# Performance work log

Hardware: AMD Instinct MI355X
Metric: run time of the kernel (lower is better)

Reference implementation:

```python
import jax, jax.numpy as jnp
import numpy as np

N = 100_000   # nodes
E = 3_200_000 # edges (avg degree 32)
IN = 256      # input feature dim


def setup_inputs() -> dict:
    key = jax.random.key(0)
    ks = jax.random.split(key, 10)
    w = lambda k, s: (jax.random.normal(k, s, jnp.float32) * 0.02)
    return {
        "x": jax.random.normal(ks[0], (N, IN), jnp.float32),
        "edge_index": jax.random.randint(ks[1], (2, E), 0, N, dtype=jnp.int32),
        "edge_attr": jax.random.normal(ks[2], (E, 1), jnp.float32),
        # conv1: ExpGraphConv(IN, 64, 128)
        "W1a": w(ks[3], (IN, 64)), "b1a": jnp.zeros((64,), jnp.float32),
        "W1b": w(ks[4], (IN + 64, 128)), "b1b": jnp.zeros((128,), jnp.float32),
        # conv2: ExpGraphConv(128, 32->hidden 64? per ctor (128, 32, 64)): msg hidden 32... kept as repo: hidden=32? Using (128,64) msg, (192,64) out per faithful cat structure
        "W2a": w(ks[5], (128, 64)), "b2a": jnp.zeros((64,), jnp.float32),
        "W2b": w(ks[6], (128 + 64, 64)), "b2b": jnp.zeros((64,), jnp.float32),
        # head
        "Wl1": w(ks[7], (64, 32)), "bl1": jnp.zeros((32,), jnp.float32),
        "Wl2": w(ks[8], (32, 1)), "bl2": jnp.zeros((1,), jnp.float32),
    }


def _mean_aggr(h, src, dst, n):
    # gather messages from source nodes, scatter-mean into destination nodes
    s = jax.ops.segment_sum(h[src], dst, num_segments=n)          # [N, d]
    cnt = jax.ops.segment_sum(jnp.ones((src.shape[0],), h.dtype), dst, num_segments=n)
    return s / jnp.maximum(cnt, 1.0)[:, None]


def _exp_graph_conv(x, src, dst, Wa, ba, Wb, bb):
    # message MLP on source features, mean aggregation, then linear on [x || aggr]
    h = x @ Wa + ba                                               # [N, hidden]
    m = _mean_aggr(h, src, dst, x.shape[0])                       # [N, hidden]
    return jnp.concatenate([x, m], axis=1) @ Wb + bb              # [N, out]


def reference(x, edge_index, edge_attr, W1a, b1a, W1b, b1b, W2a, b2a, W2b, b2b, Wl1, bl1, Wl2, bl2):
    src, dst = edge_index[0], edge_index[1]
    x = jax.nn.relu(_exp_graph_conv(x, src, dst, W1a, b1a, W1b, b1b))
    x = jax.nn.relu(_exp_graph_conv(x, src, dst, W2a, b2a, W2b, b2b))
    x = jax.nn.relu(x @ Wl1 + bl1)
    return x @ Wl2 + bl2
```

## Files before the change

kernel.cpp:

```cpp
#include <hip/hip_runtime.h>
#include <type_traits>

#define IN_DIM 256
#define CAP 10240
#define EPB 4096

typedef _Float16 f16;
typedef _Float16 f16x8 __attribute__((ext_vector_type(8)));
typedef float f32x4 __attribute__((ext_vector_type(4)));
typedef unsigned u32x4 __attribute__((ext_vector_type(4)));
typedef unsigned u32x2 __attribute__((ext_vector_type(2)));


__global__ __launch_bounds__(256) void init_cur_k(int* __restrict__ bcur) {
    int i = blockIdx.x * 256 + threadIdx.x;
    if (i < 512) bcur[i] = i * CAP;
}

__global__ __launch_bounds__(256) void bucket_scatter_k(const int* __restrict__ srcp,
                                                        const int* __restrict__ dstp,
                                                        int* __restrict__ bcur,
                                                        unsigned* __restrict__ bedge, int E) {
    __shared__ int cnt[512], lstart[512], delta[512], fill[512];
    __shared__ int pfx[256];
    __shared__ unsigned spay[EPB];
    __shared__ unsigned char sbk[EPB];
    int tid = threadIdx.x;
    cnt[tid] = 0; cnt[tid + 256] = 0;
    fill[tid] = 0; fill[tid + 256] = 0;
    __syncthreads();
    size_t base = (size_t)blockIdx.x * EPB;
    int nloc = E - (int)base; if (nloc > EPB) nloc = EPB;
    int dreg[EPB / 256], sreg[EPB / 256];
#pragma unroll
    for (int j = 0; j < EPB / 256; j++) {
        int e = j * 256 + tid;
        if (e < nloc) {
            dreg[j] = dstp[base + e];
            sreg[j] = srcp[base + e];
            atomicAdd(&cnt[dreg[j] >> 8], 1);
        }
    }
    __syncthreads();
    int a0 = cnt[2 * tid], a1 = cnt[2 * tid + 1], s = a0 + a1;
    pfx[tid] = s;
    __syncthreads();
    for (int off = 1; off < 256; off <<= 1) {
        int t2 = (tid >= off) ? pfx[tid - off] : 0;
        __syncthreads();
        pfx[tid] += t2;
        __syncthreads();
    }
    int excl = pfx[tid] - s;
    lstart[2 * tid] = excl;
    lstart[2 * tid + 1] = excl + a0;
    int g0 = 0, g1 = 0;
    if (a0) g0 = atomicAdd(&bcur[2 * tid], a0);
    if (a1) g1 = atomicAdd(&bcur[2 * tid + 1], a1);
    delta[2 * tid] = g0 - excl;
    delta[2 * tid + 1] = g1 - (excl + a0);
    __syncthreads();
#pragma unroll
    for (int j = 0; j < EPB / 256; j++) {
        int e = j * 256 + tid;
        if (e < nloc) {
            int d = dreg[j], bk = d >> 8;
            int slot = lstart[bk] + atomicAdd(&fill[bk], 1);
            spay[slot] = (unsigned)sreg[j] | ((unsigned)(d & 255) << 17);
            sbk[slot] = (unsigned char)bk;
        }
    }
    __syncthreads();
    int mid = lstart[256];
#pragma unroll
    for (int j = 0; j < EPB / 256; j++) {
        int i = j * 256 + tid;
        if (i < nloc) {
            int bk = (int)sbk[i] | ((i >= mid) ? 256 : 0);
            int gp = i + delta[bk];
            if (gp < (bk + 1) * CAP)
                bedge[gp] = spay[i];
        }
    }
}

__global__ __launch_bounds__(256) void fine_sort_k(unsigned* __restrict__ bedge,
                                                   const int* __restrict__ bcur,
                                                   int2* __restrict__ ose, int Nn) {
    __shared__ int cnt[256], cur[256], pfx[256];
    __shared__ int sorted[CAP];
    int b = blockIdx.x, tid = threadIdx.x;
    int lo = b * CAP;
    int sz = bcur[b] - lo;
    if (sz > CAP) sz = CAP;
    cnt[tid] = 0;
    __syncthreads();
    for (int i = tid; i < sz; i += 256) atomicAdd(&cnt[bedge[lo + i] >> 17], 1);
    __syncthreads();
    int c = cnt[tid];
    pfx[tid] = c;
    __syncthreads();
    for (int off = 1; off < 256; off <<= 1) {
        int t2 = (tid >= off) ? pfx[tid - off] : 0;
        __syncthreads();
        pfx[tid] += t2;
        __syncthreads();
    }
    int excl = pfx[tid] - c;
    cur[tid] = excl;
    int node = b * 256 + tid;
    if (node < Nn) ose[node] = make_int2(lo + excl, lo + excl + c);
    __syncthreads();
    for (int i = tid; i < sz; i += 256) {
        unsigned v = bedge[lo + i];
        int slot = atomicAdd(&cur[v >> 17], 1);
        sorted[slot] = (int)(v & 0x1FFFFu);
    }
    __syncthreads();
    for (int i = tid; i < sz; i += 256) bedge[lo + i] = (unsigned)sorted[i];
}


__global__ __launch_bounds__(256) void castf16_k(const float* __restrict__ X,
                                                 f16* __restrict__ Y, int n4) {
    int i = blockIdx.x * 256 + threadIdx.x;
    if (i >= n4) return;
    f32x4 v = __builtin_nontemporal_load(reinterpret_cast<const f32x4*>(X) + i);
    union { f16 h[4]; u32x2 u; } p;
    p.h[0] = (f16)v.x; p.h[1] = (f16)v.y; p.h[2] = (f16)v.z; p.h[3] = (f16)v.w;
    __builtin_nontemporal_store(p.u, reinterpret_cast<u32x2*>(Y) + i);
}

__global__ __launch_bounds__(256) void wcast_k(const float* __restrict__ W,
                                               f16* __restrict__ Wt, int K, int N) {
    int i = blockIdx.x * 256 + threadIdx.x;
    if (i >= N * K) return;
    int n = i / K, k = i - n * K;
    Wt[i] = (f16)W[(size_t)k * N + n];
}


__global__ __launch_bounds__(256) void aggr_k(const int2* __restrict__ ose,
                                              const int* __restrict__ ssrc,
                                              const f16* __restrict__ h,
                                              f16* __restrict__ m, int n) {
    int wave = (blockIdx.x * 256 + threadIdx.x) >> 6;
    int lane = threadIdx.x & 63;
    if (wave >= n) return;
    int2 se = ose[wave];
    int s0 = se.x, s1 = se.y;
    int half = lane >> 5;
    int l32 = lane & 31;
    const unsigned* h32 = reinterpret_cast<const unsigned*>(h);
    float ax = 0.f, ay = 0.f;
    for (int c = s0; c < s1; c += 64) {
        int cn = min(64, s1 - c);
        int myidx = (lane < cn) ? ssrc[c + lane] : 0;
        int t = 0;
        for (; t + 8 <= cn; t += 8) {
            int ia = __shfl(myidx, t + 0 + half);
            int ib = __shfl(myidx, t + 2 + half);
            int ic = __shfl(myidx, t + 4 + half);
            int id = __shfl(myidx, t + 6 + half);
            unsigned ua = h32[(size_t)ia * 32 + l32];
            unsigned ub = h32[(size_t)ib * 32 + l32];
            unsigned uc = h32[(size_t)ic * 32 + l32];
            unsigned ud = h32[(size_t)id * 32 + l32];
            union { unsigned u; f16 hh[2]; } qa, qb, qc, qd;
            qa.u = ua; qb.u = ub; qc.u = uc; qd.u = ud;
            ax += (float)qa.hh[0] + (float)qb.hh[0] + (float)qc.hh[0] + (float)qd.hh[0];
            ay += (float)qa.hh[1] + (float)qb.hh[1] + (float)qc.hh[1] + (float)qd.hh[1];
        }
        for (; t + 2 <= cn; t += 2) {
            int ia = __shfl(myidx, t + half);
            unsigned ua = h32[(size_t)ia * 32 + l32];
            union { unsigned u; f16 hh[2]; } qa; qa.u = ua;
            ax += (float)qa.hh[0];
            ay += (float)qa.hh[1];
        }
        if (t < cn) {
            int ia = __shfl(myidx, t);
            if (half == 0) {
                unsigned ua = h32[(size_t)ia * 32 + l32];
                union { unsigned u; f16 hh[2]; } qa; qa.u = ua;
                ax += (float)qa.hh[0];
                ay += (float)qa.hh[1];
            }
        }
    }
    ax += __shfl_xor(ax, 32);
    ay += __shfl_xor(ay, 32);
    if (half == 0) {
        float inv = 1.0f / fmaxf((float)(s1 - s0), 1.0f);
        union { unsigned u; f16 hh[2]; } q;
        q.hh[0] = (f16)(ax * inv);
        q.hh[1] = (f16)(ay * inv);
        reinterpret_cast<unsigned*>(m + (size_t)wave * 64)[l32] = q.u;
    }
}


template <int BN, bool OUT_F16>
__global__ __launch_bounds__(256) void gemm_mfma(const f16* __restrict__ A1, int K1,
                                                 const f16* __restrict__ A2, int K2,
                                                 const f16* __restrict__ Wt,
                                                 const float* __restrict__ bias,
                                                 void* __restrict__ Yv, int M, int relu,
                                                 int stream_out) {
    constexpr int BM = 64, BK = 32;
    constexpr int WN = BN / 2;
    constexpr int NB = WN / 16;
    constexpr int SEGB = BN / 64;
    using T = typename std::conditional<OUT_F16, f16, float>::type;
    constexpr int EPS = BN + 8;
    constexpr int VECN = 16 / sizeof(T);
    constexpr int TPR = BN / VECN;
    constexpr size_t SM_AB = (size_t)BM * BK * 2 + (size_t)BN * BK * 2;
    constexpr size_t SM_EP = (size_t)BM * EPS * sizeof(T);
    constexpr size_t SM = SM_AB > SM_EP ? SM_AB : SM_EP;
    __shared__ __align__(16) char smem[SM];
    f16 (*As)[BK] = reinterpret_cast<f16(*)[BK]>(smem);
    f16 (*Bs)[BK] = reinterpret_cast<f16(*)[BK]>(smem + (size_t)BM * BK * 2);
    const int tid  = threadIdx.x;
    const int wave = tid >> 6;
    const int lane = tid & 63;
    const int wr   = wave >> 1;
    const int wc   = wave & 1;
    const int quad = lane >> 4;
    const int l16  = lane & 15;
    const int row0 = blockIdx.x * BM;
    const int Ktot = K1 + K2;

    f32x4 acc[2][NB];
#pragma unroll
    for (int i = 0; i < 2; i++)
#pragma unroll
        for (int j = 0; j < NB; j++) acc[i][j] = (f32x4)(0.f);

    const int ra = tid >> 2, sa = tid & 3;
    int rowA = row0 + ra;  if (rowA >= M) rowA = M - 1;

    u32x4 aReg, bReg[SEGB];
    auto loadA = [&](int kk) {
        const f16* base; int stride, kloc;
        if (kk < K1) { base = A1; stride = K1; kloc = kk; }
        else         { base = A2; stride = K2; kloc = kk - K1; }
        aReg = __builtin_nontemporal_load(
            reinterpret_cast<const u32x4*>(base + (size_t)rowA * stride + kloc + sa * 8));
    };
    auto loadB = [&](int kk) {
#pragma unroll
        for (int i = 0; i < SEGB; i++) {
            int fid = tid + i * 256;
            int n = fid >> 2, s = fid & 3;
            bReg[i] = *reinterpret_cast<const u32x4*>(Wt + (size_t)n * Ktot + kk + s * 8);
        }
    };

    loadA(0); loadB(0);
    for (int kk = 0; kk < Ktot; kk += BK) {
        reinterpret_cast<u32x4*>(&As[0][0])[tid] = aReg;
#pragma unroll
        for (int i = 0; i < SEGB; i++)
            reinterpret_cast<u32x4*>(&Bs[0][0])[tid + i * 256] = bReg[i];
        __syncthreads();
        if (kk + BK < Ktot) { loadA(kk + BK); loadB(kk + BK); }
        f16x8 af[2], bf[NB];
#pragma unroll
        for (int rb = 0; rb < 2; rb++) {
            int row = wr * 32 + rb * 16 + l16;
            af[rb] = *reinterpret_cast<const f16x8*>(&As[row][quad * 8]);
        }
#pragma unroll
        for (int cb = 0; cb < NB; cb++) {
            int n = wc * WN + cb * 16 + l16;
            bf[cb] = *reinterpret_cast<const f16x8*>(&Bs[n][quad * 8]);
        }
#pragma unroll
        for (int rb = 0; rb < 2; rb++)
#pragma unroll
            for (int cb = 0; cb < NB; cb++)
                acc[rb][cb] = __builtin_amdgcn_mfma_f32_16x16x32_f16(af[rb], bf[cb], acc[rb][cb], 0, 0, 0);
        __syncthreads();
    }

    T* ep = reinterpret_cast<T*>(smem);
#pragma unroll
    for (int rb = 0; rb < 2; rb++) {
#pragma unroll
        for (int cb = 0; cb < NB; cb++) {
            int col = wc * WN + cb * 16 + l16;
            float bv = bias[col];
#pragma unroll
            for (int r = 0; r < 4; r++) {
                int lrow = wr * 32 + rb * 16 + quad * 4 + r;
                float v = acc[rb][cb][r] + bv;
                if (relu) v = fmaxf(v, 0.f);
                ep[(size_t)lrow * EPS + col] = (T)v;
            }
        }
    }
    __syncthreads();
#pragma unroll
    for (int p = 0; p < BM * TPR / 256; p++) {
        int fid = p * 256 + tid;
        int row = fid / TPR, c = fid % TPR;
        int grow = row0 + row;
        if (grow < M) {
            u32x4 val = *reinterpret_cast<const u32x4*>(ep + (size_t)row * EPS + c * VECN);
            u32x4* dst = reinterpret_cast<u32x4*>((T*)Yv + (size_t)grow * BN + c * VECN);
            if (stream_out) __builtin_nontemporal_store(val, dst);
            else            *dst = val;
        }
    }
}


__global__ __launch_bounds__(256) void head_k(const f16* __restrict__ x2,
                                              const float* __restrict__ Wl1,
                                              const float* __restrict__ bl1,
                                              const float* __restrict__ Wl2,
                                              const float* __restrict__ bl2,
                                              float* __restrict__ out, int n) {
    __shared__ __align__(16) float w1[64 * 32];
    __shared__ float b1s[32];
    __shared__ float w2s[32];
    for (int t = threadIdx.x; t < 2048; t += 256) w1[t] = Wl1[t];
    if (threadIdx.x < 32) {
        b1s[threadIdx.x] = bl1[threadIdx.x];
        w2s[threadIdx.x] = Wl2[threadIdx.x];
    }
    __syncthreads();
    int i = blockIdx.x * 256 + threadIdx.x;
    if (i >= n) return;
    float v[64];
    const f16x8* xr = reinterpret_cast<const f16x8*>(x2 + (size_t)i * 64);
#pragma unroll
    for (int t = 0; t < 8; t++) {
        f16x8 q = xr[t];
#pragma unroll
        for (int j = 0; j < 8; j++) v[t * 8 + j] = (float)q[j];
    }
    float hj[32];
#pragma unroll
    for (int j = 0; j < 32; j++) hj[j] = b1s[j];
    for (int k = 0; k < 64; k++) {
        float vk = v[k];
        const float4* wrow = reinterpret_cast<const float4*>(&w1[k * 32]);
#pragma unroll
        for (int j4 = 0; j4 < 8; j4++) {
            float4 wq = wrow[j4];
            hj[j4 * 4 + 0] += vk * wq.x;
            hj[j4 * 4 + 1] += vk * wq.y;
            hj[j4 * 4 + 2] += vk * wq.z;
            hj[j4 * 4 + 3] += vk * wq.w;
        }
    }
    float o = bl2[0];
#pragma unroll
    for (int j = 0; j < 32; j++) o += fmaxf(hj[j], 0.f) * w2s[j];
    out[i] = o;
}


extern "C" void kernel_launch(void* const* d_in, const int* in_sizes, int n_in,
                              void* d_out, int out_size, void* d_ws, size_t ws_size,
                              hipStream_t stream) {
    const float* x   = (const float*)d_in[0];
    const int*   ei  = (const int*)d_in[1];
    const float* W1a = (const float*)d_in[3];
    const float* b1a = (const float*)d_in[4];
    const float* W1b = (const float*)d_in[5];
    const float* b1b = (const float*)d_in[6];
    const float* W2a = (const float*)d_in[7];
    const float* b2a = (const float*)d_in[8];
    const float* W2b = (const float*)d_in[9];
    const float* b2b = (const float*)d_in[10];
    const float* Wl1 = (const float*)d_in[11];
    const float* bl1 = (const float*)d_in[12];
    const float* Wl2 = (const float*)d_in[13];
    const float* bl2 = (const float*)d_in[14];

    const int N = in_sizes[0] / IN_DIM;
    const int E = in_sizes[1] / 2;
    const int* srcp = ei;
    const int* dstp = ei + E;

    char* ws = (char*)d_ws;
    size_t off = 0;
    auto alloc = [&](size_t bytes) -> char* {
        char* p = ws + off;
        off = (off + bytes + 255) & ~(size_t)255;
        return p;
    };
    int NB2 = (N + 255) / 256;
    int*      bcur  = (int*)alloc(512 * 4);
    unsigned* bedge = (unsigned*)alloc((size_t)NB2 * CAP * 4);
    int2*     ose   = (int2*)alloc((size_t)N * 8);
    f16*      x16   = (f16*)alloc((size_t)N * IN_DIM * 2);
    f16*      hbuf  = (f16*)alloc((size_t)N * 64 * 2);
    f16*      mbuf  = (f16*)alloc((size_t)N * 64 * 2);
    f16*      x1    = (f16*)alloc((size_t)N * 128 * 2);
    f16*      h2    = (f16*)alloc((size_t)N * 64 * 2);
    f16*      Wt1a  = (f16*)alloc(256 * 64 * 2);
    f16*      Wt1b  = (f16*)alloc(320 * 128 * 2);
    f16*      Wt2a  = (f16*)alloc(128 * 64 * 2);
    f16*      Wt2b  = (f16*)alloc(192 * 64 * 2);
    (void)ws_size;

    init_cur_k<<<2, 256, 0, stream>>>(bcur);
    int ebk = (E + EPB - 1) / EPB;
    bucket_scatter_k<<<ebk, 256, 0, stream>>>(srcp, dstp, bcur, bedge, E);
    fine_sort_k<<<NB2, 256, 0, stream>>>(bedge, bcur, ose, N);

    int n4 = N * IN_DIM / 4;
    castf16_k<<<(n4 + 255) / 256, 256, 0, stream>>>(x, x16, n4);
    wcast_k<<<(256 * 64 + 255) / 256, 256, 0, stream>>>(W1a, Wt1a, 256, 64);
    wcast_k<<<(320 * 128 + 255) / 256, 256, 0, stream>>>(W1b, Wt1b, 320, 128);
    wcast_k<<<(128 * 64 + 255) / 256, 256, 0, stream>>>(W2a, Wt2a, 128, 64);
    wcast_k<<<(192 * 64 + 255) / 256, 256, 0, stream>>>(W2b, Wt2b, 192, 64);

    int mb = (N + 63) / 64;
    int ab = (N * 64 + 255) / 256;

    gemm_mfma<64, true><<<mb, 256, 0, stream>>>(x16, IN_DIM, nullptr, 0, Wt1a, b1a, hbuf, N, 0, 0);
    aggr_k<<<ab, 256, 0, stream>>>(ose, (const int*)bedge, hbuf, mbuf, N);
    gemm_mfma<128, true><<<mb, 256, 0, stream>>>(x16, IN_DIM, mbuf, 64, Wt1b, b1b, x1, N, 1, 1);

    gemm_mfma<64, true><<<mb, 256, 0, stream>>>(x1, 128, nullptr, 0, Wt2a, b2a, hbuf, N, 0, 0);
    aggr_k<<<ab, 256, 0, stream>>>(ose, (const int*)bedge, hbuf, mbuf, N);
    gemm_mfma<64, true><<<mb, 256, 0, stream>>>(x1, 128, mbuf, 64, Wt2b, b2b, h2, N, 1, 1);

    head_k<<<(N + 255) / 256, 256, 0, stream>>>(h2, Wl1, bl1, Wl2, bl2, (float*)d_out, N);
}
```

Baseline: 478.1 us.

## Fuse x cast into GEMMs, head into last GEMM, widen aggregation loads

Drops the standalone fp32-to-fp16 cast of x; the two layer-1 GEMMs now read fp32 x directly and convert it in registers. The MLP head is folded into the epilogue of the final GEMM, which removes the h2 buffer and the head kernel. The four weight casts become one kernel, the bucket-cursor init becomes a memset with bucket offsets folded into delta, and aggregation uses 8-byte loads across four row groups. The cost is that x (fp32) is read twice at twice the byte width instead of once plus two fp16 passes, and the fused head adds serial per-thread work to the GEMM epilogue.

Result: faster. 439.3 us (-8.1%).

```diff
diff --git a/kernel.cpp b/kernel.cpp
--- a/kernel.cpp
+++ b/kernel.cpp
@@ -1,5 +1,4 @@
 #include <hip/hip_runtime.h>
-#include <type_traits>
 
 #define IN_DIM 256
 #define CAP 10240
@@ -11,11 +10,6 @@
 typedef unsigned u32x4 __attribute__((ext_vector_type(4)));
 typedef unsigned u32x2 __attribute__((ext_vector_type(2)));
 
-
-__global__ __launch_bounds__(256) void init_cur_k(int* __restrict__ bcur) {
-    int i = blockIdx.x * 256 + threadIdx.x;
-    if (i < 512) bcur[i] = i * CAP;
-}
 
 __global__ __launch_bounds__(256) void bucket_scatter_k(const int* __restrict__ srcp,
                                                         const int* __restrict__ dstp,
@@ -57,8 +51,8 @@
     int g0 = 0, g1 = 0;
     if (a0) g0 = atomicAdd(&bcur[2 * tid], a0);
     if (a1) g1 = atomicAdd(&bcur[2 * tid + 1], a1);
-    delta[2 * tid] = g0 - excl;
-    delta[2 * tid + 1] = g1 - (excl + a0);
+    delta[2 * tid]     = (2 * tid) * CAP + g0 - excl;
+    delta[2 * tid + 1] = (2 * tid + 1) * CAP + g1 - (excl + a0);
     __syncthreads();
 #pragma unroll
     for (int j = 0; j < EPB / 256; j++) {
@@ -91,7 +85,7 @@
     __shared__ int sorted[CAP];
     int b = blockIdx.x, tid = threadIdx.x;
     int lo = b * CAP;
-    int sz = bcur[b] - lo;
+    int sz = bcur[b];
     if (sz > CAP) sz = CAP;
     cnt[tid] = 0;
     __syncthreads();
@@ -121,22 +115,19 @@
 }
 
 
-__global__ __launch_bounds__(256) void castf16_k(const float* __restrict__ X,
-                                                 f16* __restrict__ Y, int n4) {
+__global__ __launch_bounds__(256) void wcast_all_k(const float* __restrict__ W1a, f16* __restrict__ Wt1a,
+                                                   const float* __restrict__ W1b, f16* __restrict__ Wt1b,
+                                                   const float* __restrict__ W2a, f16* __restrict__ Wt2a,
+                                                   const float* __restrict__ W2b, f16* __restrict__ Wt2b) {
     int i = blockIdx.x * 256 + threadIdx.x;
-    if (i >= n4) return;
-    f32x4 v = __builtin_nontemporal_load(reinterpret_cast<const f32x4*>(X) + i);
-    union { f16 h[4]; u32x2 u; } p;
-    p.h[0] = (f16)v.x; p.h[1] = (f16)v.y; p.h[2] = (f16)v.z; p.h[3] = (f16)v.w;
-    __builtin_nontemporal_store(p.u, reinterpret_cast<u32x2*>(Y) + i);
-}
-
-__global__ __launch_bounds__(256) void wcast_k(const float* __restrict__ W,
-                                               f16* __restrict__ Wt, int K, int N) {
-    int i = blockIdx.x * 256 + threadIdx.x;
-    if (i >= N * K) return;
-    int n = i / K, k = i - n * K;
-    Wt[i] = (f16)W[(size_t)k * N + n];
+    const float* W; f16* Wt; int K, N, local;
+    if (i < 16384)      { W = W1a; Wt = Wt1a; K = 256; N = 64;  local = i; }
+    else if (i < 57344) { W = W1b; Wt = Wt1b; K = 320; N = 128; local = i - 16384; }
+    else if (i < 65536) { W = W2a; Wt = Wt2a; K = 128; N = 64;  local = i - 57344; }
+    else if (i < 77824) { W = W2b; Wt = Wt2b; K = 192; N = 64;  local = i - 65536; }
+    else return;
+    int n = local / K, k = local - n * K;
+    Wt[local] = (f16)W[(size_t)k * N + n];
 }
 
 
@@ -149,75 +140,75 @@
     if (wave >= n) return;
     int2 se = ose[wave];
     int s0 = se.x, s1 = se.y;
-    int half = lane >> 5;
-    int l32 = lane & 31;
-    const unsigned* h32 = reinterpret_cast<const unsigned*>(h);
-    float ax = 0.f, ay = 0.f;
+    int q = lane >> 4, l16 = lane & 15;
+    const u32x2* hp = reinterpret_cast<const u32x2*>(h);
+    float a0 = 0.f, a1 = 0.f, a2 = 0.f, a3 = 0.f;
+    auto acc = [&](u32x2 u) {
+        union { u32x2 u; f16 hh[4]; } p; p.u = u;
+        a0 += (float)p.hh[0]; a1 += (float)p.hh[1];
+        a2 += (float)p.hh[2]; a3 += (float)p.hh[3];
+    };
     for (int c = s0; c < s1; c += 64) {
         int cn = min(64, s1 - c);
         int myidx = (lane < cn) ? ssrc[c + lane] : 0;
         int t = 0;
-        for (; t + 8 <= cn; t += 8) {
-            int ia = __shfl(myidx, t + 0 + half);
-            int ib = __shfl(myidx, t + 2 + half);
-            int ic = __shfl(myidx, t + 4 + half);
-            int id = __shfl(myidx, t + 6 + half);
-            unsigned ua = h32[(size_t)ia * 32 + l32];
-            unsigned ub = h32[(size_t)ib * 32 + l32];
-            unsigned uc = h32[(size_t)ic * 32 + l32];
-            unsigned ud = h32[(size_t)id * 32 + l32];
-            union { unsigned u; f16 hh[2]; } qa, qb, qc, qd;
-            qa.u = ua; qb.u = ub; qc.u = uc; qd.u = ud;
-            ax += (float)qa.hh[0] + (float)qb.hh[0] + (float)qc.hh[0] + (float)qd.hh[0];
-            ay += (float)qa.hh[1] + (float)qb.hh[1] + (float)qc.hh[1] + (float)qd.hh[1];
-        }
-        for (; t + 2 <= cn; t += 2) {
-            int ia = __shfl(myidx, t + half);
-            unsigned ua = h32[(size_t)ia * 32 + l32];
-            union { unsigned u; f16 hh[2]; } qa; qa.u = ua;
-            ax += (float)qa.hh[0];
-            ay += (float)qa.hh[1];
-        }
-        if (t < cn) {
-            int ia = __shfl(myidx, t);
-            if (half == 0) {
-                unsigned ua = h32[(size_t)ia * 32 + l32];
-                union { unsigned u; f16 hh[2]; } qa; qa.u = ua;
-                ax += (float)qa.hh[0];
-                ay += (float)qa.hh[1];
-            }
-        }
-    }
-    ax += __shfl_xor(ax, 32);
-    ay += __shfl_xor(ay, 32);
-    if (half == 0) {
+        for (; t + 16 <= cn; t += 16) {
+            int ia = __shfl(myidx, t + q);
+            int ib = __shfl(myidx, t + 4 + q);
+            int ic = __shfl(myidx, t + 8 + q);
+            int id = __shfl(myidx, t + 12 + q);
+            u32x2 ua = hp[(size_t)ia * 16 + l16];
+            u32x2 ub = hp[(size_t)ib * 16 + l16];
+            u32x2 uc = hp[(size_t)ic * 16 + l16];
+            u32x2 ud = hp[(size_t)id * 16 + l16];
+            acc(ua); acc(ub); acc(uc); acc(ud);
+        }
+        for (; t < cn; t += 4) {
+            int r = t + q;
+            int rr = (r < cn) ? r : (cn - 1);
+            int ia = __shfl(myidx, rr);
+            if (r < cn) acc(hp[(size_t)ia * 16 + l16]);
+        }
+    }
+    a0 += __shfl_xor(a0, 16); a1 += __shfl_xor(a1, 16);
+    a2 += __shfl_xor(a2, 16); a3 += __shfl_xor(a3, 16);
+    a0 += __shfl_xor(a0, 32); a1 += __shfl_xor(a1, 32);
+    a2 += __shfl_xor(a2, 32); a3 += __shfl_xor(a3, 32);
+    if (lane < 16) {
         float inv = 1.0f / fmaxf((float)(s1 - s0), 1.0f);
-        union { unsigned u; f16 hh[2]; } q;
-        q.hh[0] = (f16)(ax * inv);
-        q.hh[1] = (f16)(ay * inv);
-        reinterpret_cast<unsigned*>(m + (size_t)wave * 64)[l32] = q.u;
-    }
-}
-
-
-template <int BN, bool OUT_F16>
-__global__ __launch_bounds__(256) void gemm_mfma(const f16* __restrict__ A1, int K1,
+        union { u32x2 u; f16 hh[4]; } p;
+        p.hh[0] = (f16)(a0 * inv); p.hh[1] = (f16)(a1 * inv);
+        p.hh[2] = (f16)(a2 * inv); p.hh[3] = (f16)(a3 * inv);
+        reinterpret_cast<u32x2*>(m + (size_t)wave * 64)[l16] = p.u;
+    }
+}
+
+
+template <int BN, bool A1F32, bool FUSE_HEAD>
+__global__ __launch_bounds__(256) void gemm_mfma(const void* __restrict__ A1v, int K1,
                                                  const f16* __restrict__ A2, int K2,
                                                  const f16* __restrict__ Wt,
                                                  const float* __restrict__ bias,
-                                                 void* __restrict__ Yv, int M, int relu,
-                                                 int stream_out) {
+                                                 f16* __restrict__ Y, int M, int relu,
+                                                 int stream_out,
+                                                 const float* __restrict__ Wl1,
+                                                 const float* __restrict__ bl1,
+                                                 const float* __restrict__ Wl2,
+                                                 const float* __restrict__ bl2,
+                                                 float* __restrict__ out) {
+    static_assert(!FUSE_HEAD || BN == 64, "head fusion assumes BN==64");
     constexpr int BM = 64, BK = 32;
     constexpr int WN = BN / 2;
     constexpr int NB = WN / 16;
     constexpr int SEGB = BN / 64;
-    using T = typename std::conditional<OUT_F16, f16, float>::type;
     constexpr int EPS = BN + 8;
-    constexpr int VECN = 16 / sizeof(T);
+    constexpr int VECN = 8;
     constexpr int TPR = BN / VECN;
     constexpr size_t SM_AB = (size_t)BM * BK * 2 + (size_t)BN * BK * 2;
-    constexpr size_t SM_EP = (size_t)BM * EPS * sizeof(T);
-    constexpr size_t SM = SM_AB > SM_EP ? SM_AB : SM_EP;
+    constexpr size_t SM_EP = (size_t)BM * EPS * 2;
+    constexpr size_t SM_HEAD = FUSE_HEAD ? (2048 * 4 + 64 * 4) : 0;
+    constexpr size_t SM1 = SM_EP + SM_HEAD;
+    constexpr size_t SM = SM_AB > SM1 ? SM_AB : SM1;
     __shared__ __align__(16) char smem[SM];
     f16 (*As)[BK] = reinterpret_cast<f16(*)[BK]>(smem);
     f16 (*Bs)[BK] = reinterpret_cast<f16(*)[BK]>(smem + (size_t)BM * BK * 2);
@@ -231,6 +222,12 @@
     const int row0 = blockIdx.x * BM;
     const int Ktot = K1 + K2;
 
+    if constexpr (FUSE_HEAD) {
+        float* w1s = reinterpret_cast<float*>(smem + SM_EP);
+        for (int t2 = tid; t2 < 2048; t2 += 256) w1s[t2] = Wl1[t2];
+        if (tid < 32) { (w1s + 2048)[tid] = bl1[tid]; (w1s + 2048 + 32)[tid] = Wl2[tid]; }
+    }
+
     f32x4 acc[2][NB];
 #pragma unroll
     for (int i = 0; i < 2; i++)
@@ -242,11 +239,24 @@
 
     u32x4 aReg, bReg[SEGB];
     auto loadA = [&](int kk) {
-        const f16* base; int stride, kloc;
-        if (kk < K1) { base = A1; stride = K1; kloc = kk; }
-        else         { base = A2; stride = K2; kloc = kk - K1; }
-        aReg = __builtin_nontemporal_load(
-            reinterpret_cast<const u32x4*>(base + (size_t)rowA * stride + kloc + sa * 8));
+        if (kk < K1) {
+            if constexpr (A1F32) {
+                const float* bp = reinterpret_cast<const float*>(A1v) +
+                                  (size_t)rowA * K1 + kk + sa * 8;
+                f32x4 v0 = __builtin_nontemporal_load(reinterpret_cast<const f32x4*>(bp));
+                f32x4 v1 = __builtin_nontemporal_load(reinterpret_cast<const f32x4*>(bp) + 1);
+                union { f16 h[8]; u32x4 u; } p;
+                p.h[0] = (f16)v0.x; p.h[1] = (f16)v0.y; p.h[2] = (f16)v0.z; p.h[3] = (f16)v0.w;
+                p.h[4] = (f16)v1.x; p.h[5] = (f16)v1.y; p.h[6] = (f16)v1.z; p.h[7] = (f16)v1.w;
+                aReg = p.u;
+            } else {
+                aReg = __builtin_nontemporal_load(reinterpret_cast<const u32x4*>(
+                    reinterpret_cast<const f16*>(A1v) + (size_t)rowA * K1 + kk + sa * 8));
+            }
+        } else {
+            aReg = __builtin_nontemporal_load(reinterpret_cast<const u32x4*>(
+                A2 + (size_t)rowA * K2 + (kk - K1) + sa * 8));
+        }
     };
     auto loadB = [&](int kk) {
 #pragma unroll
@@ -284,7 +294,7 @@
         __syncthreads();
     }
 
-    T* ep = reinterpret_cast<T*>(smem);
+    f16* ep = reinterpret_cast<f16*>(smem);
 #pragma unroll
     for (int rb = 0; rb < 2; rb++) {
 #pragma unroll
@@ -296,70 +306,48 @@
                 int lrow = wr * 32 + rb * 16 + quad * 4 + r;
                 float v = acc[rb][cb][r] + bv;
                 if (relu) v = fmaxf(v, 0.f);
-                ep[(size_t)lrow * EPS + col] = (T)v;
+                ep[(size_t)lrow * EPS + col] = (f16)v;
             }
         }
     }
     __syncthreads();
-#pragma unroll
-    for (int p = 0; p < BM * TPR / 256; p++) {
-        int fid = p * 256 + tid;
-        int row = fid / TPR, c = fid % TPR;
+
+    if constexpr (FUSE_HEAD) {
+        float* w1s = reinterpret_cast<float*>(smem + SM_EP);
+        float* b1s = w1s + 2048;
+        float* w2s = b1s + 32;
+        int row = tid >> 2, part = tid & 3;
+        const f16* eprow = ep + (size_t)row * EPS;
+        float hj[8];
+#pragma unroll
+        for (int j = 0; j < 8; j++) hj[j] = b1s[part * 8 + j];
+        for (int k = 0; k < 64; k++) {
+            float v = (float)eprow[k];
+            const float* wrow = &w1s[k * 32 + part * 8];
+#pragma unroll
+            for (int j = 0; j < 8; j++) hj[j] += v * wrow[j];
+        }
+        float o = 0.f;
+#pragma unroll
+        for (int j = 0; j < 8; j++) o += fmaxf(hj[j], 0.f) * w2s[part * 8 + j];
+        o += __shfl_xor(o, 1);
+        o += __shfl_xor(o, 2);
         int grow = row0 + row;
-        if (grow < M) {
-            u32x4 val = *reinterpret_cast<const u32x4*>(ep + (size_t)row * EPS + c * VECN);
-            u32x4* dst = reinterpret_cast<u32x4*>((T*)Yv + (size_t)grow * BN + c * VECN);
-            if (stream_out) __builtin_nontemporal_store(val, dst);
-            else            *dst = val;
-        }
-    }
-}
-
-
-__global__ __launch_bounds__(256) void head_k(const f16* __restrict__ x2,
-                                              const float* __restrict__ Wl1,
-                                              const float* __restrict__ bl1,
-                                              const float* __restrict__ Wl2,
-                                              const float* __restrict__ bl2,
-                                              float* __restrict__ out, int n) {
-    __shared__ __align__(16) float w1[64 * 32];
-    __shared__ float b1s[32];
-    __shared__ float w2s[32];
-    for (int t = threadIdx.x; t < 2048; t += 256) w1[t] = Wl1[t];
-    if (threadIdx.x < 32) {
-        b1s[threadIdx.x] = bl1[threadIdx.x];
-        w2s[threadIdx.x] = Wl2[threadIdx.x];
-    }
-    __syncthreads();
-    int i = blockIdx.x * 256 + threadIdx.x;
-    if (i >= n) return;
-    float v[64];
-    const f16x8* xr = reinterpret_cast<const f16x8*>(x2 + (size_t)i * 64);
-#pragma unroll
-    for (int t = 0; t < 8; t++) {
-        f16x8 q = xr[t];
-#pragma unroll
-        for (int j = 0; j < 8; j++) v[t * 8 + j] = (float)q[j];
-    }
-    float hj[32];
-#pragma unroll
-    for (int j = 0; j < 32; j++) hj[j] = b1s[j];
-    for (int k = 0; k < 64; k++) {
-        float vk = v[k];
-        const float4* wrow = reinterpret_cast<const float4*>(&w1[k * 32]);
-#pragma unroll
-        for (int j4 = 0; j4 < 8; j4++) {
-            float4 wq = wrow[j4];
-            hj[j4 * 4 + 0] += vk * wq.x;
-            hj[j4 * 4 + 1] += vk * wq.y;
-            hj[j4 * 4 + 2] += vk * wq.z;
-            hj[j4 * 4 + 3] += vk * wq.w;
-        }
-    }
-    float o = bl2[0];
-#pragma unroll
-    for (int j = 0; j < 32; j++) o += fmaxf(hj[j], 0.f) * w2s[j];
-    out[i] = o;
+        if (part == 0 && grow < M) out[grow] = o + bl2[0];
+    } else {
+#pragma unroll
+        for (int p = 0; p < BM * TPR / 256; p++) {
+            int fid = p * 256 + tid;
+            int row = fid / TPR, c = fid % TPR;
+            int grow = row0 + row;
+            if (grow < M) {
+                u32x4 val = *reinterpret_cast<const u32x4*>(ep + (size_t)row * EPS + c * VECN);
+                u32x4* dst = reinterpret_cast<u32x4*>(Y + (size_t)grow * BN + c * VECN);
+                if (stream_out) __builtin_nontemporal_store(val, dst);
+                else            *dst = val;
+            }
+        }
+    }
 }
 
 
@@ -397,39 +385,39 @@
     int*      bcur  = (int*)alloc(512 * 4);
     unsigned* bedge = (unsigned*)alloc((size_t)NB2 * CAP * 4);
     int2*     ose   = (int2*)alloc((size_t)N * 8);
-    f16*      x16   = (f16*)alloc((size_t)N * IN_DIM * 2);
     f16*      hbuf  = (f16*)alloc((size_t)N * 64 * 2);
     f16*      mbuf  = (f16*)alloc((size_t)N * 64 * 2);
     f16*      x1    = (f16*)alloc((size_t)N * 128 * 2);
-    f16*      h2    = (f16*)alloc((size_t)N * 64 * 2);
     f16*      Wt1a  = (f16*)alloc(256 * 64 * 2);
     f16*      Wt1b  = (f16*)alloc(320 * 128 * 2);
     f16*      Wt2a  = (f16*)alloc(128 * 64 * 2);
     f16*      Wt2b  = (f16*)alloc(192 * 64 * 2);
     (void)ws_size;
 
-    init_cur_k<<<2, 256, 0, stream>>>(bcur);
+    hipMemsetAsync(bcur, 0, 512 * 4, stream);
     int ebk = (E + EPB - 1) / EPB;
     bucket_scatter_k<<<ebk, 256, 0, stream>>>(srcp, dstp, bcur, bedge, E);
     fine_sort_k<<<NB2, 256, 0, stream>>>(bedge, bcur, ose, N);
 
-    int n4 = N * IN_DIM / 4;
-    castf16_k<<<(n4 + 255) / 256, 256, 0, stream>>>(x, x16, n4);
-    wcast_k<<<(256 * 64 + 255) / 256, 256, 0, stream>>>(W1a, Wt1a, 256, 64);
-    wcast_k<<<(320 * 128 + 255) / 256, 256, 0, stream>>>(W1b, Wt1b, 320, 128);
-    wcast_k<<<(128 * 64 + 255) / 256, 256, 0, stream>>>(W2a, Wt2a, 128, 64);
-    wcast_k<<<(192 * 64 + 255) / 256, 256, 0, stream>>>(W2b, Wt2b, 192, 64);
+    wcast_all_k<<<304, 256, 0, stream>>>(W1a, Wt1a, W1b, Wt1b, W2a, Wt2a, W2b, Wt2b);
 
     int mb = (N + 63) / 64;
     int ab = (N * 64 + 255) / 256;
 
-    gemm_mfma<64, true><<<mb, 256, 0, stream>>>(x16, IN_DIM, nullptr, 0, Wt1a, b1a, hbuf, N, 0, 0);
+    gemm_mfma<64, true, false><<<mb, 256, 0, stream>>>(
+        x, IN_DIM, nullptr, 0, Wt1a, b1a, hbuf, N, 0, 0,
+        nullptr, nullptr, nullptr, nullptr, nullptr);
     aggr_k<<<ab, 256, 0, stream>>>(ose, (const int*)bedge, hbuf, mbuf, N);
-    gemm_mfma<128, true><<<mb, 256, 0, stream>>>(x16, IN_DIM, mbuf, 64, Wt1b, b1b, x1, N, 1, 1);
-
-    gemm_mfma<64, true><<<mb, 256, 0, stream>>>(x1, 128, nullptr, 0, Wt2a, b2a, hbuf, N, 0, 0);
+    gemm_mfma<128, true, false><<<mb, 256, 0, stream>>>(
+        x, IN_DIM, mbuf, 64, Wt1b, b1b, x1, N, 1, 1,
+        nullptr, nullptr, nullptr, nullptr, nullptr);
+
+    gemm_mfma<64, false, false><<<mb, 256, 0, stream>>>(
+        x1, 128, nullptr, 0, Wt2a, b2a, hbuf, N, 0, 0,
+        nullptr, nullptr, nullptr, nullptr, nullptr);
     aggr_k<<<ab, 256, 0, stream>>>(ose, (const int*)bedge, hbuf, mbuf, N);
-    gemm_mfma<64, true><<<mb, 256, 0, stream>>>(x1, 128, mbuf, 64, Wt2b, b2b, h2, N, 1, 1);
-
-    head_k<<<(N + 255) / 256, 256, 0, stream>>>(h2, Wl1, bl1, Wl2, bl2, (float*)d_out, N);
-}
+
+    gemm_mfma<64, false, true><<<mb, 256, 0, stream>>>(
+        x1, 128, mbuf, 64, Wt2b, b2b, nullptr, N, 1, 0,
+        Wl1, bl1, Wl2, bl2, (float*)d_out);
+}
```
